# Kernel tuning notes

Measured on AMD Instinct MI355X. Metric: run time of the kernel, lower is better.

## Reference

```python
import jax, jax.numpy as jnp
import numpy as np

N_NODES = 50000
N_EDGES = 800000
N_FEAT = 128
N_HIDDEN = 128
N_CLASSES = 64


def sage_mean_conv(x, src, dst, W_self, W_neigh, b, n_nodes):
    # DGL SAGEConv (mean): out = x @ W_self + mean_neigh(x) @ W_neigh + b
    # mean over in-neighbors: messages flow src -> dst
    msg = x[src]  # [E, F] gather
    h_sum = jax.ops.segment_sum(msg, dst, num_segments=n_nodes)  # [N, F]
    deg = jax.ops.segment_sum(jnp.ones((src.shape[0],), x.dtype), dst,
                              num_segments=n_nodes)
    h_mean = h_sum / jnp.maximum(deg, 1.0)[:, None]
    return x @ W_self + h_mean @ W_neigh + b


def setup_inputs() -> dict:
    key = jax.random.key(0)
    ks = jax.random.split(key, 8)
    sc1 = 1.0 / np.sqrt(N_FEAT)
    sc2 = 1.0 / np.sqrt(N_HIDDEN)
    return {
        "x": jax.random.normal(ks[0], (N_NODES, N_FEAT), jnp.float32),
        "W_self1": jax.random.normal(ks[1], (N_FEAT, N_HIDDEN), jnp.float32) * sc1,
        "W_neigh1": jax.random.normal(ks[2], (N_FEAT, N_HIDDEN), jnp.float32) * sc1,
        "b1": jnp.zeros((N_HIDDEN,), jnp.float32),
        "W_self2": jax.random.normal(ks[3], (N_HIDDEN, N_CLASSES), jnp.float32) * sc2,
        "W_neigh2": jax.random.normal(ks[4], (N_HIDDEN, N_CLASSES), jnp.float32) * sc2,
        "b2": jnp.zeros((N_CLASSES,), jnp.float32),
        "src": jax.random.randint(ks[5], (N_EDGES,), 0, N_NODES, jnp.int32),
        "dst": jax.random.randint(ks[6], (N_EDGES,), 0, N_NODES, jnp.int32),
    }


def reference(x, W_self1, W_neigh1, b1, W_self2, W_neigh2, b2, src, dst):
    n = x.shape[0]
    h = sage_mean_conv(x, src, dst, W_self1, W_neigh1, b1, n)
    h = jax.nn.relu(h)
    logits = sage_mean_conv(h, src, dst, W_self2, W_neigh2, b2, n)
    return logits
```

## Files before the change

kernel.cpp:

```cpp
#include <hip/hip_runtime.h>
#include <hip/hip_fp16.h>

#define N_NODES 50000
#define N_EDGES 800000
#define N_FEAT 128
#define N_HIDDEN 128
#define N_CLASSES 64

#define NBUCK 512
#define BUCK_NODES 98
#define BIN_CHUNK 2048
#define BIN_BLK ((N_EDGES + BIN_CHUNK - 1) / BIN_CHUNK)

#define PACK1_BLK 16
#define PACK2_BLK 8
#define PREP_BLK (BIN_BLK + PACK1_BLK + PACK2_BLK)
#define GEMM1_BLK ((N_NODES + 31) / 32)
#define BG_BLK (BIN_BLK + GEMM1_BLK)

typedef __attribute__((ext_vector_type(8))) short bf16x8;
typedef __attribute__((ext_vector_type(4))) float f32x4;
typedef __attribute__((ext_vector_type(2))) float f32x2;

__device__ __forceinline__ unsigned short f32_to_bf16(float f) {
    unsigned int u = __float_as_uint(f);
    return (unsigned short)((u + 0x7fffu + ((u >> 16) & 1u)) >> 16);
}
__device__ __forceinline__ float bf16lo(unsigned int v) { return __uint_as_float(v << 16); }
__device__ __forceinline__ float bf16hi(unsigned int v) { return __uint_as_float(v & 0xffff0000u); }

#if defined(__has_builtin)
#if __has_builtin(__builtin_amdgcn_cvt_pk_f32_fp8) && __has_builtin(__builtin_amdgcn_cvt_pk_fp8_f32)
#define FP8_HW 1
#endif
#endif

__device__ __forceinline__ unsigned char f32_to_fp8(float f) {
#ifdef FP8_HW
    return (unsigned char)(__builtin_amdgcn_cvt_pk_fp8_f32(f, f, 0, false) & 0xff);
#else
    unsigned short hb = __half_as_ushort(__float2half(f));
    return (unsigned char)((hb + 0x7fu + ((hb >> 8) & 1u)) >> 8);
#endif
}

__device__ __forceinline__ void fp8x4_to_f32(unsigned int u, float* o) {
#ifdef FP8_HW
    f32x2 lo = __builtin_amdgcn_cvt_pk_f32_fp8(u, false);
    f32x2 hi = __builtin_amdgcn_cvt_pk_f32_fp8(u, true);
    o[0] = lo.x; o[1] = lo.y; o[2] = hi.x; o[3] = hi.y;
#else
    o[0] = __half2float(__ushort_as_half((unsigned short)((u & 0xffu) << 8)));
    o[1] = __half2float(__ushort_as_half((unsigned short)(((u >> 8) & 0xffu) << 8)));
    o[2] = __half2float(__ushort_as_half((unsigned short)(((u >> 16) & 0xffu) << 8)));
    o[3] = __half2float(__ushort_as_half((unsigned short)(((u >> 24) & 0xffu) << 8)));
#endif
}

template <int NOUT>
__device__ void pack_w_body(int idx, const float* __restrict__ Wself,
                            const float* __restrict__ Wneigh,
                            unsigned short* __restrict__ Bp) {
    constexpr int NT = NOUT / 16;
    constexpr int NO = NOUT / 2;
    if (idx >= 4 * NT * 64) return;
    const int lane = idx & 63;
    const int tc = idx >> 6;
    const int c = tc % NT;
    const int t = tc / NT;
    const int n = c * 16 + (lane & 15);
    const int k0 = t * 32 + (lane >> 4) * 8;
    const float* W = (n < NO) ? Wself : Wneigh;
    const int nn = (n < NO) ? n : n - NO;
    ushort4 lo, hi;
    lo.x = f32_to_bf16(W[(k0 + 0) * NO + nn]);
    lo.y = f32_to_bf16(W[(k0 + 1) * NO + nn]);
    lo.z = f32_to_bf16(W[(k0 + 2) * NO + nn]);
    lo.w = f32_to_bf16(W[(k0 + 3) * NO + nn]);
    hi.x = f32_to_bf16(W[(k0 + 4) * NO + nn]);
    hi.y = f32_to_bf16(W[(k0 + 5) * NO + nn]);
    hi.z = f32_to_bf16(W[(k0 + 6) * NO + nn]);
    hi.w = f32_to_bf16(W[(k0 + 7) * NO + nn]);
    ((ushort4*)&Bp[(size_t)idx * 8])[0] = lo;
    ((ushort4*)&Bp[(size_t)idx * 8])[1] = hi;
}

__device__ void a0_body(int blk, const int* __restrict__ dst, int* __restrict__ hists) {
    __shared__ int h[NBUCK];
    const int t = threadIdx.x;
    h[t] = 0;
    h[t + 256] = 0;
    __syncthreads();
    const int lo = blk * BIN_CHUNK;
    const int hi = min(lo + BIN_CHUNK, N_EDGES);
    for (int i4 = (lo >> 2) + t; i4 < (hi >> 2); i4 += 256) {
        int4 d = ((const int4*)dst)[i4];
        atomicAdd(&h[d.x / BUCK_NODES], 1);
        atomicAdd(&h[d.y / BUCK_NODES], 1);
        atomicAdd(&h[d.z / BUCK_NODES], 1);
        atomicAdd(&h[d.w / BUCK_NODES], 1);
    }
    __syncthreads();
    hists[blk * NBUCK + t] = h[t];
    hists[blk * NBUCK + t + 256] = h[t + 256];
}

__global__ __launch_bounds__(256) void prep_kernel(
        const int* __restrict__ dst, int* __restrict__ hists,
        const float* __restrict__ Ws1, const float* __restrict__ Wn1,
        unsigned short* __restrict__ Bp1,
        const float* __restrict__ Ws2, const float* __restrict__ Wn2,
        unsigned short* __restrict__ Bp2) {
    const int b = blockIdx.x;
    const int t = threadIdx.x;
    if (b < BIN_BLK) {
        a0_body(b, dst, hists);
    } else if (b < BIN_BLK + PACK1_BLK) {
        int idx = (b - BIN_BLK) * 256 + t;
        pack_w_body<256>(idx, Ws1, Wn1, Bp1);
    } else {
        int idx = (b - BIN_BLK - PACK1_BLK) * 256 + t;
        pack_w_body<128>(idx, Ws2, Wn2, Bp2);
    }
}

__global__ __launch_bounds__(64) void colsum_kernel(const int* __restrict__ hists,
                                                    int* __restrict__ colsum) {
    const int b = blockIdx.x;
    const int t = threadIdx.x;
    int v = 0;
    for (int c = t; c < BIN_BLK; c += 64) v += hists[c * NBUCK + b];
#pragma unroll
    for (int s = 32; s > 0; s >>= 1) v += __shfl_down(v, s);
    if (t == 0) colsum[b] = v;
}

__global__ __launch_bounds__(512) void bscan_kernel(const int* __restrict__ colsum,
                                                    int* __restrict__ bstart,
                                                    int* __restrict__ bcursor) {
    __shared__ int sc[NBUCK];
    const int t = threadIdx.x;
    const int v = colsum[t];
    sc[t] = v;
    __syncthreads();
    for (int s = 1; s < NBUCK; s <<= 1) {
        int u = (t >= s) ? sc[t - s] : 0;
        __syncthreads();
        sc[t] += u;
        __syncthreads();
    }
    const int excl = sc[t] - v;
    bstart[t] = excl;
    bcursor[t] = excl;
    if (t == NBUCK - 1) bstart[NBUCK] = sc[t];
}

__device__ void a1_body(int blk, const int* __restrict__ src, const int* __restrict__ dst,
                        const int* __restrict__ hists,
                        int* __restrict__ bcursor, unsigned int* __restrict__ binned) {
    __shared__ int base[NBUCK];
    __shared__ int cnt[NBUCK];
    const int t = threadIdx.x;
    {
        const int h0 = hists[blk * NBUCK + t];
        const int h1 = hists[blk * NBUCK + t + 256];
        base[t] = atomicAdd(&bcursor[t], h0);
        base[t + 256] = atomicAdd(&bcursor[t + 256], h1);
        cnt[t] = 0;
        cnt[t + 256] = 0;
    }
    __syncthreads();
    const int lo = blk * BIN_CHUNK;
    const int hi = min(lo + BIN_CHUNK, N_EDGES);
    for (int i4 = (lo >> 2) + t; i4 < (hi >> 2); i4 += 256) {
        int4 d = ((const int4*)dst)[i4];
        int4 s = ((const int4*)src)[i4];
#pragma unroll
        for (int j = 0; j < 4; ++j) {
            const int dj = (j == 0) ? d.x : (j == 1) ? d.y : (j == 2) ? d.z : d.w;
            const int sj = (j == 0) ? s.x : (j == 1) ? s.y : (j == 2) ? s.z : s.w;
            const int b = dj / BUCK_NODES;
            const int r = atomicAdd(&cnt[b], 1);
            binned[base[b] + r] = ((unsigned int)(dj - b * BUCK_NODES) << 16) | (unsigned int)sj;
        }
    }
}

__device__ __forceinline__ bf16x8 load_a_f32(const float* base) {
    float4 u = ((const float4*)base)[0];
    float4 v = ((const float4*)base)[1];
    bf16x8 a;
    a[0] = (short)f32_to_bf16(u.x); a[1] = (short)f32_to_bf16(u.y);
    a[2] = (short)f32_to_bf16(u.z); a[3] = (short)f32_to_bf16(u.w);
    a[4] = (short)f32_to_bf16(v.x); a[5] = (short)f32_to_bf16(v.y);
    a[6] = (short)f32_to_bf16(v.z); a[7] = (short)f32_to_bf16(v.w);
    return a;
}

template <int NOUT, bool AF32, bool SB16, bool PFP8>
__device__ void gemm_mfma_body(int gblk,
                               const float* __restrict__ af,
                               const unsigned short* __restrict__ ab,
                               const unsigned short* __restrict__ Bp,
                               const float* __restrict__ bias,
                               float* __restrict__ s32,
                               unsigned short* __restrict__ s16,
                               unsigned char* __restrict__ p8,
                               unsigned short* __restrict__ p16) {
    constexpr int NT = NOUT / 16;
    constexpr int NO = NOUT / 2;
    constexpr int NSUB = NT / 4;

    const int tid = threadIdx.x;
    const int wave = tid >> 6;
    const int lane = tid & 63;
    const int mcol = lane & 15;
    const int kgrp = lane >> 4;

    const int mbase = gblk * 32;
    int r0 = mbase + mcol;       if (r0 >= N_NODES) r0 = N_NODES - 1;
    int r1 = mbase + 16 + mcol;  if (r1 >= N_NODES) r1 = N_NODES - 1;

    f32x4 acc[2][NSUB];
#pragma unroll
    for (int mt = 0; mt < 2; ++mt)
#pragma unroll
        for (int c = 0; c < NSUB; ++c)
            acc[mt][c] = (f32x4){0.f, 0.f, 0.f, 0.f};

#pragma unroll
    for (int t = 0; t < 4; ++t) {
        bf16x8 a0, a1;
        if (AF32) {
            a0 = load_a_f32(&af[(size_t)r0 * 128 + t * 32 + kgrp * 8]);
            a1 = load_a_f32(&af[(size_t)r1 * 128 + t * 32 + kgrp * 8]);
        } else {
            a0 = *(const bf16x8*)&ab[(size_t)r0 * 128 + t * 32 + kgrp * 8];
            a1 = *(const bf16x8*)&ab[(size_t)r1 * 128 + t * 32 + kgrp * 8];
        }
#pragma unroll
        for (int c = 0; c < NSUB; ++c) {
            const int ct = wave * NSUB + c;
            bf16x8 bfrag = *(const bf16x8*)&Bp[((size_t)(t * NT + ct) * 64 + lane) * 8];
            acc[0][c] = __builtin_amdgcn_mfma_f32_16x16x32_bf16(a0, bfrag, acc[0][c], 0, 0, 0);
            acc[1][c] = __builtin_amdgcn_mfma_f32_16x16x32_bf16(a1, bfrag, acc[1][c], 0, 0, 0);
        }
    }

    float bv[NSUB];
    int ncols[NSUB];
#pragma unroll
    for (int c = 0; c < NSUB; ++c) {
        ncols[c] = (wave * NSUB + c) * 16 + mcol;
        bv[c] = (ncols[c] < NO) ? bias[ncols[c]] : 0.f;
    }

#pragma unroll
    for (int mt = 0; mt < 2; ++mt) {
#pragma unroll
        for (int c = 0; c < NSUB; ++c) {
            const int ncol = ncols[c];
#pragma unroll
            for (int r = 0; r < 4; ++r) {
                const int node = mbase + mt * 16 + kgrp * 4 + r;
                if (node >= N_NODES) continue;
                const float v = acc[mt][c][r];
                if (ncol < NO) {
                    if (SB16) s16[(size_t)node * NO + ncol] = f32_to_bf16(v + bv[c]);
                    else      s32[(size_t)node * NO + ncol] = v + bv[c];
                } else if (PFP8) {
                    p8[(size_t)node * NO + (ncol - NO)] = f32_to_fp8(v);
                } else {
                    p16[(size_t)node * NO + (ncol - NO)] = f32_to_bf16(v);
                }
            }
        }
    }
}

__global__ __launch_bounds__(256) void bin_gemm1_kernel(
        const int* __restrict__ src, const int* __restrict__ dst,
        const int* __restrict__ hists,
        int* __restrict__ bcursor, unsigned int* __restrict__ binned,
        const float* __restrict__ x,
        const unsigned short* __restrict__ Bp1,
        const float* __restrict__ b1,
        unsigned short* __restrict__ s1, unsigned char* __restrict__ p1) {
    const int b = blockIdx.x;
    if (b < BIN_BLK) {
        a1_body(b, src, dst, hists, bcursor, binned);
    } else {
        gemm_mfma_body<256, true, true, true>(b - BIN_BLK, x, nullptr, Bp1, b1,
                                              nullptr, s1, p1, nullptr);
    }
}

__global__ __launch_bounds__(256) void bucket_build_kernel(
        const unsigned int* __restrict__ binned,
        const int* __restrict__ bstart,
        int* __restrict__ offsets,
        unsigned short* __restrict__ csr16) {
    __shared__ int cnt[128];
    __shared__ int pre[128];
    const int b = blockIdx.x;
    const int t = threadIdx.x;
    const int n0 = b * BUCK_NODES;
    const int nn = min(N_NODES - n0, BUCK_NODES);
    const int e0 = bstart[b];
    const int e1 = bstart[b + 1];

    if (t < 128) cnt[t] = 0;
    __syncthreads();
    for (int i = e0 + t; i < e1; i += 256) {
        atomicAdd(&cnt[binned[i] >> 16], 1);
    }
    __syncthreads();
    if (t < 128) {
        pre[t] = cnt[t];
    }
    __syncthreads();
    for (int s = 1; s < 128; s <<= 1) {
        int u = (t < 128 && t >= s) ? pre[t - s] : 0;
        __syncthreads();
        if (t < 128) pre[t] += u;
        __syncthreads();
    }
    if (t < 128) {
        const int excl = pre[t] - cnt[t];
        if (t < nn) offsets[n0 + t] = e0 + excl;
        pre[t] = excl;
        cnt[t] = 0;
    }
    if (b == 0 && t == 0) offsets[N_NODES] = N_EDGES;
    __syncthreads();
    for (int i = e0 + t; i < e1; i += 256) {
        const unsigned int u = binned[i];
        const int dl = (int)(u >> 16);
        const int r = atomicAdd(&cnt[dl], 1);
        csr16[e0 + pre[dl] + r] = (unsigned short)(u & 0xffffu);
    }
}

__global__ __launch_bounds__(256) void gemm2_kernel(
        const unsigned short* __restrict__ h1b,
        const unsigned short* __restrict__ Bp2,
        const float* __restrict__ b2,
        float* __restrict__ s2, unsigned short* __restrict__ p2) {
    gemm_mfma_body<128, false, false, false>(blockIdx.x, nullptr, h1b, Bp2, b2,
                                             s2, nullptr, nullptr, p2);
}

__global__ __launch_bounds__(256) void agg_relu_128_kernel(
        const unsigned short* __restrict__ s16,
        const unsigned char* __restrict__ p,
        const int* __restrict__ offsets,
        const unsigned short* __restrict__ csr16,
        unsigned short* __restrict__ h1b) {
    const int wave = threadIdx.x >> 6;
    const int lane = threadIdx.x & 63;
    const int q = lane >> 4;
    const int l = lane & 15;
    const int node = blockIdx.x * 4 + wave;
    if (node >= N_NODES) return;

    const int off0 = offsets[node];
    const int off1 = offsets[node + 1];
    const uint2* pp = (const uint2*)p;

    float a[8];
#pragma unroll
    for (int k = 0; k < 8; ++k) a[k] = 0.f;

    for (int i = off0 + q; i < off1; i += 32) {
        int idx[8];
        float m[8];
        uint2 w[8];
#pragma unroll
        for (int j = 0; j < 8; ++j) {
            const int e = i + 4 * j;
            const int ec = min(e, off1 - 1);
            idx[j] = (int)csr16[ec];
            m[j] = (e < off1) ? 1.f : 0.f;
        }
#pragma unroll
        for (int j = 0; j < 8; ++j) w[j] = pp[(size_t)idx[j] * 16 + l];
#pragma unroll
        for (int j = 0; j < 8; ++j) {
            float d0[4], d1[4];
            fp8x4_to_f32(w[j].x, d0);
            fp8x4_to_f32(w[j].y, d1);
            a[0] += m[j] * d0[0]; a[1] += m[j] * d0[1];
            a[2] += m[j] * d0[2]; a[3] += m[j] * d0[3];
            a[4] += m[j] * d1[0]; a[5] += m[j] * d1[1];
            a[6] += m[j] * d1[2]; a[7] += m[j] * d1[3];
        }
    }
#pragma unroll
    for (int k = 0; k < 8; ++k) {
        a[k] += __shfl_xor(a[k], 16);
        a[k] += __shfl_xor(a[k], 32);
    }

    if (q == 0) {
        const float invdeg = 1.0f / fmaxf((float)(off1 - off0), 1.0f);
        uint4 sw = ((const uint4*)s16)[(size_t)node * 16 + l];
        float sf[8];
        sf[0] = bf16lo(sw.x); sf[1] = bf16hi(sw.x);
        sf[2] = bf16lo(sw.y); sf[3] = bf16hi(sw.y);
        sf[4] = bf16lo(sw.z); sf[5] = bf16hi(sw.z);
        sf[6] = bf16lo(sw.w); sf[7] = bf16hi(sw.w);
        ushort4 o0, o1;
        o0.x = f32_to_bf16(fmaxf(sf[0] + a[0] * invdeg, 0.f));
        o0.y = f32_to_bf16(fmaxf(sf[1] + a[1] * invdeg, 0.f));
        o0.z = f32_to_bf16(fmaxf(sf[2] + a[2] * invdeg, 0.f));
        o0.w = f32_to_bf16(fmaxf(sf[3] + a[3] * invdeg, 0.f));
        o1.x = f32_to_bf16(fmaxf(sf[4] + a[4] * invdeg, 0.f));
        o1.y = f32_to_bf16(fmaxf(sf[5] + a[5] * invdeg, 0.f));
        o1.z = f32_to_bf16(fmaxf(sf[6] + a[6] * invdeg, 0.f));
        o1.w = f32_to_bf16(fmaxf(sf[7] + a[7] * invdeg, 0.f));
        ((ushort4*)h1b)[(size_t)node * 32 + l * 2] = o0;
        ((ushort4*)h1b)[(size_t)node * 32 + l * 2 + 1] = o1;
    }
}

__global__ __launch_bounds__(256) void agg_64_kernel(
        const unsigned short* __restrict__ p,
        const int* __restrict__ offsets,
        const unsigned short* __restrict__ csr16,
        float* __restrict__ out) {
    const int wave = threadIdx.x >> 6;
    const int lane = threadIdx.x & 63;
    const int st = lane >> 3;
    const int l = lane & 7;
    const int node = blockIdx.x * 4 + wave;
    if (node >= N_NODES) return;

    const int off0 = offsets[node];
    const int off1 = offsets[node + 1];
    const uint4* pp = (const uint4*)p;

    float a[8];
#pragma unroll
    for (int k = 0; k < 8; ++k) a[k] = 0.f;

    for (int i = off0 + st; i < off1; i += 32) {
        int idx[4];
        float m[4];
        uint4 w[4];
#pragma unroll
        for (int j = 0; j < 4; ++j) {
            const int e = i + 8 * j;
            const int ec = min(e, off1 - 1);
            idx[j] = (int)csr16[ec];
            m[j] = (e < off1) ? 1.f : 0.f;
        }
#pragma unroll
        for (int j = 0; j < 4; ++j) w[j] = pp[(size_t)idx[j] * 8 + l];
#pragma unroll
        for (int j = 0; j < 4; ++j) {
            a[0] += m[j] * bf16lo(w[j].x); a[1] += m[j] * bf16hi(w[j].x);
            a[2] += m[j] * bf16lo(w[j].y); a[3] += m[j] * bf16hi(w[j].y);
            a[4] += m[j] * bf16lo(w[j].z); a[5] += m[j] * bf16hi(w[j].z);
            a[6] += m[j] * bf16lo(w[j].w); a[7] += m[j] * bf16hi(w[j].w);
        }
    }
#pragma unroll
    for (int k = 0; k < 8; ++k) {
        a[k] += __shfl_xor(a[k], 8);
        a[k] += __shfl_xor(a[k], 16);
        a[k] += __shfl_xor(a[k], 32);
    }

    if (st == 0) {
        const float invdeg = 1.0f / fmaxf((float)(off1 - off0), 1.0f);
        float4 s0 = ((float4*)out)[(size_t)node * 16 + l * 2];
        float4 s1 = ((float4*)out)[(size_t)node * 16 + l * 2 + 1];
        s0.x += a[0] * invdeg; s0.y += a[1] * invdeg;
        s0.z += a[2] * invdeg; s0.w += a[3] * invdeg;
        s1.x += a[4] * invdeg; s1.y += a[5] * invdeg;
        s1.z += a[6] * invdeg; s1.w += a[7] * invdeg;
        ((float4*)out)[(size_t)node * 16 + l * 2] = s0;
        ((float4*)out)[(size_t)node * 16 + l * 2 + 1] = s1;
    }
}

extern "C" void kernel_launch(void* const* d_in, const int* in_sizes, int n_in,
                              void* d_out, int out_size, void* d_ws, size_t ws_size,
                              hipStream_t stream) {
    const float* x        = (const float*)d_in[0];
    const float* W_self1  = (const float*)d_in[1];
    const float* W_neigh1 = (const float*)d_in[2];
    const float* b1       = (const float*)d_in[3];
    const float* W_self2  = (const float*)d_in[4];
    const float* W_neigh2 = (const float*)d_in[5];
    const float* b2       = (const float*)d_in[6];
    const int*   src      = (const int*)d_in[7];
    const int*   dst      = (const int*)d_in[8];
    float* out = (float*)d_out;

    int* bstart  = (int*)d_ws;
    int* bcursor = bstart + 544;
    int* colsum  = bcursor + 512;
    int* offsets = colsum + 512;
    int* hists   = offsets + 50048;
    unsigned int* binned = (unsigned int*)(hists + BIN_BLK * NBUCK);
    unsigned short* csr16 = (unsigned short*)(binned + 800000);
    unsigned short* Bp1 = csr16 + 800000;
    unsigned short* Bp2 = Bp1 + 32768;
    unsigned short* s1  = Bp2 + 16384;
    unsigned short* h1b = s1 + (size_t)N_NODES * 128;
    unsigned char* p1   = (unsigned char*)(h1b + (size_t)N_NODES * 128);
    unsigned short* p2  = (unsigned short*)p1;

    prep_kernel<<<PREP_BLK, 256, 0, stream>>>(dst, hists,
                                              W_self1, W_neigh1, Bp1,
                                              W_self2, W_neigh2, Bp2);
    colsum_kernel<<<NBUCK, 64, 0, stream>>>(hists, colsum);
    bscan_kernel<<<1, NBUCK, 0, stream>>>(colsum, bstart, bcursor);
    bin_gemm1_kernel<<<BG_BLK, 256, 0, stream>>>(src, dst, hists, bcursor, binned,
                                                 x, Bp1, b1, s1, p1);
    bucket_build_kernel<<<NBUCK, 256, 0, stream>>>(binned, bstart, offsets, csr16);
    agg_relu_128_kernel<<<(N_NODES + 3) / 4, 256, 0, stream>>>(s1, p1, offsets, csr16, h1b);
    gemm2_kernel<<<(N_NODES + 31) / 32, 256, 0, stream>>>(h1b, Bp2, b2, out, p2);
    agg_64_kernel<<<(N_NODES + 3) / 4, 256, 0, stream>>>(p2, offsets, csr16, out);
}
```

Measured before the change: 196.7 us.

## Fuse layer-1 aggregation+ReLU with layer-2 GEMM via shared-memory tile

```diff
diff --git a/kernel.cpp b/kernel.cpp
--- a/kernel.cpp
+++ b/kernel.cpp
@@ -17,6 +17,8 @@
 #define PREP_BLK (BIN_BLK + PACK1_BLK + PACK2_BLK)
 #define GEMM1_BLK ((N_NODES + 31) / 32)
 #define BG_BLK (BIN_BLK + GEMM1_BLK)
+
+#define AG_LDW 136
 
 typedef __attribute__((ext_vector_type(8))) short bf16x8;
 typedef __attribute__((ext_vector_type(4))) float f32x4;
@@ -197,19 +199,13 @@
     return a;
 }
 
-template <int NOUT, bool AF32, bool SB16, bool PFP8>
-__device__ void gemm_mfma_body(int gblk,
-                               const float* __restrict__ af,
-                               const unsigned short* __restrict__ ab,
-                               const unsigned short* __restrict__ Bp,
-                               const float* __restrict__ bias,
-                               float* __restrict__ s32,
-                               unsigned short* __restrict__ s16,
-                               unsigned char* __restrict__ p8,
-                               unsigned short* __restrict__ p16) {
-    constexpr int NT = NOUT / 16;
-    constexpr int NO = NOUT / 2;
-    constexpr int NSUB = NT / 4;
+__device__ void gemm1_body(int gblk,
+                           const float* __restrict__ x,
+                           const unsigned short* __restrict__ Bp,
+                           const float* __restrict__ bias,
+                           unsigned short* __restrict__ s16,
+                           unsigned char* __restrict__ p8) {
+    constexpr int NT = 16, NO = 128, NSUB = 4;
 
     const int tid = threadIdx.x;
     const int wave = tid >> 6;
@@ -230,14 +226,8 @@
 
 #pragma unroll
     for (int t = 0; t < 4; ++t) {
-        bf16x8 a0, a1;
-        if (AF32) {
-            a0 = load_a_f32(&af[(size_t)r0 * 128 + t * 32 + kgrp * 8]);
-            a1 = load_a_f32(&af[(size_t)r1 * 128 + t * 32 + kgrp * 8]);
-        } else {
-            a0 = *(const bf16x8*)&ab[(size_t)r0 * 128 + t * 32 + kgrp * 8];
-            a1 = *(const bf16x8*)&ab[(size_t)r1 * 128 + t * 32 + kgrp * 8];
-        }
+        bf16x8 a0 = load_a_f32(&x[(size_t)r0 * 128 + t * 32 + kgrp * 8]);
+        bf16x8 a1 = load_a_f32(&x[(size_t)r1 * 128 + t * 32 + kgrp * 8]);
 #pragma unroll
         for (int c = 0; c < NSUB; ++c) {
             const int ct = wave * NSUB + c;
@@ -265,14 +255,8 @@
                 const int node = mbase + mt * 16 + kgrp * 4 + r;
                 if (node >= N_NODES) continue;
                 const float v = acc[mt][c][r];
-                if (ncol < NO) {
-                    if (SB16) s16[(size_t)node * NO + ncol] = f32_to_bf16(v + bv[c]);
-                    else      s32[(size_t)node * NO + ncol] = v + bv[c];
-                } else if (PFP8) {
-                    p8[(size_t)node * NO + (ncol - NO)] = f32_to_fp8(v);
-                } else {
-                    p16[(size_t)node * NO + (ncol - NO)] = f32_to_bf16(v);
-                }
+                if (ncol < NO) s16[(size_t)node * NO + ncol] = f32_to_bf16(v + bv[c]);
+                else           p8[(size_t)node * NO + (ncol - NO)] = f32_to_fp8(v);
             }
         }
     }
@@ -290,8 +274,7 @@
     if (b < BIN_BLK) {
         a1_body(b, src, dst, hists, bcursor, binned);
     } else {
-        gemm_mfma_body<256, true, true, true>(b - BIN_BLK, x, nullptr, Bp1, b1,
-                                              nullptr, s1, p1, nullptr);
+        gemm1_body(b - BIN_BLK, x, Bp1, b1, s1, p1);
     }
 }
 
@@ -315,9 +298,7 @@
         atomicAdd(&cnt[binned[i] >> 16], 1);
     }
     __syncthreads();
-    if (t < 128) {
-        pre[t] = cnt[t];
-    }
+    if (t < 128) pre[t] = cnt[t];
     __syncthreads();
     for (int s = 1; s < 128; s <<= 1) {
         int u = (t < 128 && t >= s) ? pre[t - s] : 0;
@@ -341,85 +322,136 @@
     }
 }
 
-__global__ __launch_bounds__(256) void gemm2_kernel(
-        const unsigned short* __restrict__ h1b,
-        const unsigned short* __restrict__ Bp2,
-        const float* __restrict__ b2,
-        float* __restrict__ s2, unsigned short* __restrict__ p2) {
-    gemm_mfma_body<128, false, false, false>(blockIdx.x, nullptr, h1b, Bp2, b2,
-                                             s2, nullptr, nullptr, p2);
-}
-
-__global__ __launch_bounds__(256) void agg_relu_128_kernel(
+__global__ __launch_bounds__(256) void agg1_gemm2_kernel(
         const unsigned short* __restrict__ s16,
         const unsigned char* __restrict__ p,
         const int* __restrict__ offsets,
         const unsigned short* __restrict__ csr16,
-        unsigned short* __restrict__ h1b) {
-    const int wave = threadIdx.x >> 6;
-    const int lane = threadIdx.x & 63;
+        const unsigned short* __restrict__ Bp2,
+        const float* __restrict__ b2,
+        float* __restrict__ out,
+        unsigned short* __restrict__ p2) {
+    __shared__ unsigned short hl[32 * AG_LDW];
+    const int tid = threadIdx.x;
+    const int wave = tid >> 6;
+    const int lane = tid & 63;
     const int q = lane >> 4;
     const int l = lane & 15;
-    const int node = blockIdx.x * 4 + wave;
-    if (node >= N_NODES) return;
-
-    const int off0 = offsets[node];
-    const int off1 = offsets[node + 1];
+    const int mbase = blockIdx.x * 32;
     const uint2* pp = (const uint2*)p;
 
-    float a[8];
-#pragma unroll
-    for (int k = 0; k < 8; ++k) a[k] = 0.f;
-
-    for (int i = off0 + q; i < off1; i += 32) {
-        int idx[8];
-        float m[8];
-        uint2 w[8];
-#pragma unroll
-        for (int j = 0; j < 8; ++j) {
-            const int e = i + 4 * j;
-            const int ec = min(e, off1 - 1);
-            idx[j] = (int)csr16[ec];
-            m[j] = (e < off1) ? 1.f : 0.f;
-        }
-#pragma unroll
-        for (int j = 0; j < 8; ++j) w[j] = pp[(size_t)idx[j] * 16 + l];
-#pragma unroll
-        for (int j = 0; j < 8; ++j) {
-            float d0[4], d1[4];
-            fp8x4_to_f32(w[j].x, d0);
-            fp8x4_to_f32(w[j].y, d1);
-            a[0] += m[j] * d0[0]; a[1] += m[j] * d0[1];
-            a[2] += m[j] * d0[2]; a[3] += m[j] * d0[3];
-            a[4] += m[j] * d1[0]; a[5] += m[j] * d1[1];
-            a[6] += m[j] * d1[2]; a[7] += m[j] * d1[3];
-        }
-    }
-#pragma unroll
-    for (int k = 0; k < 8; ++k) {
-        a[k] += __shfl_xor(a[k], 16);
-        a[k] += __shfl_xor(a[k], 32);
-    }
-
-    if (q == 0) {
-        const float invdeg = 1.0f / fmaxf((float)(off1 - off0), 1.0f);
-        uint4 sw = ((const uint4*)s16)[(size_t)node * 16 + l];
-        float sf[8];
-        sf[0] = bf16lo(sw.x); sf[1] = bf16hi(sw.x);
-        sf[2] = bf16lo(sw.y); sf[3] = bf16hi(sw.y);
-        sf[4] = bf16lo(sw.z); sf[5] = bf16hi(sw.z);
-        sf[6] = bf16lo(sw.w); sf[7] = bf16hi(sw.w);
-        ushort4 o0, o1;
-        o0.x = f32_to_bf16(fmaxf(sf[0] + a[0] * invdeg, 0.f));
-        o0.y = f32_to_bf16(fmaxf(sf[1] + a[1] * invdeg, 0.f));
-        o0.z = f32_to_bf16(fmaxf(sf[2] + a[2] * invdeg, 0.f));
-        o0.w = f32_to_bf16(fmaxf(sf[3] + a[3] * invdeg, 0.f));
-        o1.x = f32_to_bf16(fmaxf(sf[4] + a[4] * invdeg, 0.f));
-        o1.y = f32_to_bf16(fmaxf(sf[5] + a[5] * invdeg, 0.f));
-        o1.z = f32_to_bf16(fmaxf(sf[6] + a[6] * invdeg, 0.f));
-        o1.w = f32_to_bf16(fmaxf(sf[7] + a[7] * invdeg, 0.f));
-        ((ushort4*)h1b)[(size_t)node * 32 + l * 2] = o0;
-        ((ushort4*)h1b)[(size_t)node * 32 + l * 2 + 1] = o1;
+    for (int pass = 0; pass < 8; ++pass) {
+        const int slot = pass * 4 + wave;
+        const int node = mbase + slot;
+        if (node < N_NODES) {
+            const int off0 = offsets[node];
+            const int off1 = offsets[node + 1];
+            float a[8];
+#pragma unroll
+            for (int k = 0; k < 8; ++k) a[k] = 0.f;
+
+            for (int i = off0 + q; i < off1; i += 32) {
+                int idx[8];
+                float m[8];
+                uint2 w[8];
+#pragma unroll
+                for (int j = 0; j < 8; ++j) {
+                    const int e = i + 4 * j;
+                    const int ec = min(e, off1 - 1);
+                    idx[j] = (int)csr16[ec];
+                    m[j] = (e < off1) ? 1.f : 0.f;
+                }
+#pragma unroll
+                for (int j = 0; j < 8; ++j) w[j] = pp[(size_t)idx[j] * 16 + l];
+#pragma unroll
+                for (int j = 0; j < 8; ++j) {
+                    float d0[4], d1[4];
+                    fp8x4_to_f32(w[j].x, d0);
+                    fp8x4_to_f32(w[j].y, d1);
+                    a[0] += m[j] * d0[0]; a[1] += m[j] * d0[1];
+                    a[2] += m[j] * d0[2]; a[3] += m[j] * d0[3];
+                    a[4] += m[j] * d1[0]; a[5] += m[j] * d1[1];
+                    a[6] += m[j] * d1[2]; a[7] += m[j] * d1[3];
+                }
+            }
+#pragma unroll
+            for (int k = 0; k < 8; ++k) {
+                a[k] += __shfl_xor(a[k], 16);
+                a[k] += __shfl_xor(a[k], 32);
+            }
+
+            if (q == 0) {
+                const float invdeg = 1.0f / fmaxf((float)(off1 - off0), 1.0f);
+                uint4 sw = ((const uint4*)s16)[(size_t)node * 16 + l];
+                float sf[8];
+                sf[0] = bf16lo(sw.x); sf[1] = bf16hi(sw.x);
+                sf[2] = bf16lo(sw.y); sf[3] = bf16hi(sw.y);
+                sf[4] = bf16lo(sw.z); sf[5] = bf16hi(sw.z);
+                sf[6] = bf16lo(sw.w); sf[7] = bf16hi(sw.w);
+                ushort4 o0, o1;
+                o0.x = f32_to_bf16(fmaxf(sf[0] + a[0] * invdeg, 0.f));
+                o0.y = f32_to_bf16(fmaxf(sf[1] + a[1] * invdeg, 0.f));
+                o0.z = f32_to_bf16(fmaxf(sf[2] + a[2] * invdeg, 0.f));
+                o0.w = f32_to_bf16(fmaxf(sf[3] + a[3] * invdeg, 0.f));
+                o1.x = f32_to_bf16(fmaxf(sf[4] + a[4] * invdeg, 0.f));
+                o1.y = f32_to_bf16(fmaxf(sf[5] + a[5] * invdeg, 0.f));
+                o1.z = f32_to_bf16(fmaxf(sf[6] + a[6] * invdeg, 0.f));
+                o1.w = f32_to_bf16(fmaxf(sf[7] + a[7] * invdeg, 0.f));
+                *(ushort4*)&hl[slot * AG_LDW + l * 8] = o0;
+                *(ushort4*)&hl[slot * AG_LDW + l * 8 + 4] = o1;
+            }
+        }
+    }
+    __syncthreads();
+
+    {
+        constexpr int NT = 8, NO = 64, NSUB = 2;
+        const int mcol = lane & 15;
+        const int kgrp = lane >> 4;
+
+        f32x4 acc[2][NSUB];
+#pragma unroll
+        for (int mt = 0; mt < 2; ++mt)
+#pragma unroll
+            for (int c = 0; c < NSUB; ++c)
+                acc[mt][c] = (f32x4){0.f, 0.f, 0.f, 0.f};
+
+#pragma unroll
+        for (int t = 0; t < 4; ++t) {
+            bf16x8 a0 = *(const bf16x8*)&hl[mcol * AG_LDW + t * 32 + kgrp * 8];
+            bf16x8 a1 = *(const bf16x8*)&hl[(16 + mcol) * AG_LDW + t * 32 + kgrp * 8];
+#pragma unroll
+            for (int c = 0; c < NSUB; ++c) {
+                const int ct = wave * NSUB + c;
+                bf16x8 bfrag = *(const bf16x8*)&Bp2[((size_t)(t * NT + ct) * 64 + lane) * 8];
+                acc[0][c] = __builtin_amdgcn_mfma_f32_16x16x32_bf16(a0, bfrag, acc[0][c], 0, 0, 0);
+                acc[1][c] = __builtin_amdgcn_mfma_f32_16x16x32_bf16(a1, bfrag, acc[1][c], 0, 0, 0);
+            }
+        }
+
+        float bv[NSUB];
+        int ncols[NSUB];
+#pragma unroll
+        for (int c = 0; c < NSUB; ++c) {
+            ncols[c] = (wave * NSUB + c) * 16 + mcol;
+            bv[c] = (ncols[c] < NO) ? b2[ncols[c]] : 0.f;
+        }
+
+#pragma unroll
+        for (int mt = 0; mt < 2; ++mt) {
+#pragma unroll
+            for (int c = 0; c < NSUB; ++c) {
+                const int ncol = ncols[c];
+#pragma unroll
+                for (int r = 0; r < 4; ++r) {
+                    const int node = mbase + mt * 16 + kgrp * 4 + r;
+                    if (node >= N_NODES) continue;
+                    const float v = acc[mt][c][r];
+                    if (ncol < NO) out[(size_t)node * NO + ncol] = v + bv[c];
+                    else           p2[(size_t)node * NO + (ncol - NO)] = f32_to_bf16(v);
+                }
+            }
+        }
     }
 }
 
@@ -508,9 +540,8 @@
     unsigned short* Bp1 = csr16 + 800000;
     unsigned short* Bp2 = Bp1 + 32768;
     unsigned short* s1  = Bp2 + 16384;
-    unsigned short* h1b = s1 + (size_t)N_NODES * 128;
-    unsigned char* p1   = (unsigned char*)(h1b + (size_t)N_NODES * 128);
-    unsigned short* p2  = (unsigned short*)p1;
+    unsigned char* p1   = (unsigned char*)(s1 + (size_t)N_NODES * 128);
+    unsigned short* p2  = (unsigned short*)(p1 + (size_t)N_NODES * 128);
 
     prep_kernel<<<PREP_BLK, 256, 0, stream>>>(dst, hists,
                                               W_self1, W_neigh1, Bp1,
@@ -520,7 +551,7 @@
     bin_gemm1_kernel<<<BG_BLK, 256, 0, stream>>>(src, dst, hists, bcursor, binned,
                                                  x, Bp1, b1, s1, p1);
     bucket_build_kernel<<<NBUCK, 256, 0, stream>>>(binned, bstart, offsets, csr16);
-    agg_relu_128_kernel<<<(N_NODES + 3) / 4, 256, 0, stream>>>(s1, p1, offsets, csr16, h1b);
-    gemm2_kernel<<<(N_NODES + 31) / 32, 256, 0, stream>>>(h1b, Bp2, b2, out, p2);
+    agg1_gemm2_kernel<<<(N_NODES + 31) / 32, 256, 0, stream>>>(
+        s1, p1, offsets, csr16, Bp2, b2, out, p2);
     agg_64_kernel<<<(N_NODES + 3) / 4, 256, 0, stream>>>(p2, offsets, csr16, out);
 }
```

Result: no change. 199.8 us (+1.6%).
